# Performance work log

Hardware: AMD Instinct MI355X
Metric: run time of the kernel (lower is better)

The kernel has to match this reference:

```python
import jax, jax.numpy as jnp
import numpy as np

N_NODES = 100000
N_EDGES = 3200000
IN_FEAT = 512
HIDDEN = 256
N_CLASS = 40


def setup_inputs() -> dict:
    key = jax.random.key(0)
    ks = jax.random.split(key, 6)
    x = jax.random.normal(ks[0], (N_NODES, IN_FEAT), dtype=jnp.float32)
    w1 = jax.random.uniform(ks[1], (IN_FEAT, HIDDEN), dtype=jnp.float32)
    b1 = jnp.zeros((HIDDEN,), dtype=jnp.float32)
    w2 = jax.random.uniform(ks[2], (HIDDEN, N_CLASS), dtype=jnp.float32)
    b2 = jnp.zeros((N_CLASS,), dtype=jnp.float32)
    edge_val = jax.random.uniform(ks[3], (N_EDGES,), dtype=jnp.float32)
    edge_row = jax.random.randint(ks[4], (N_EDGES,), 0, N_NODES, dtype=jnp.int32)
    edge_col = jax.random.randint(ks[5], (N_EDGES,), 0, N_NODES, dtype=jnp.int32)
    return {"x": x, "w1": w1, "b1": b1, "w2": w2, "b2": b2,
            "edge_val": edge_val, "edge_row": edge_row, "edge_col": edge_col}


def _graph_conv(h, w, b, edge_val, edge_row, edge_col, n_nodes):
    # dense transform: [N, d_in] @ [d_in, d_out]
    support = h @ w
    # sparse adj @ support via gather + segment_sum (COO SpMM)
    msgs = edge_val[:, None] * support[edge_col]          # [E, d_out]
    agg = jax.ops.segment_sum(msgs, edge_row, num_segments=n_nodes)
    return agg + b


def reference(x, w1, b1, w2, b2, edge_val, edge_row, edge_col):
    n = x.shape[0]
    h = jax.nn.relu(_graph_conv(x, w1, b1, edge_val, edge_row, edge_col, n))
    # dropout is identity in eval mode (training=False)
    out = _graph_conv(h, w2, b2, edge_val, edge_row, edge_col, n)
    return jax.nn.log_softmax(out, axis=1)
```

## Files before the change

kernel.cpp:

```cpp
#include <hip/hip_runtime.h>
#include <cstdint>
#include <cstddef>

#define N_NODES 100000
#define N_EDGES 3200000
#define IN_FEAT 512
#define HIDDEN  256
#define N_CLASS 40

#define N_BUCKETS 196
#define SC_CHUNK 4096
#define N_SC_BLOCKS 782

#define OFF_SUPPORT1 ((size_t)0)
#define OFF_H        ((size_t)51200000)
#define OFF_SUPPORT2 ((size_t)102400000)
#define OFF_W1T      ((size_t)118400000)
#define OFF_RPTR     ((size_t)118662144)
#define OFF_BCNT     ((size_t)119062272)
#define OFF_BBASE    ((size_t)119063296)
#define OFF_BCUR     ((size_t)119064320)
#define OFF_BINNED   ((size_t)119065344)
#define OFF_SEDGE    ((size_t)144665344)

typedef __attribute__((ext_vector_type(8))) short short8x;
typedef __attribute__((ext_vector_type(4))) float f32x4;

static __device__ __forceinline__ unsigned short f2bf(float f) {
  unsigned u = __float_as_uint(f);
  unsigned r = (u + 0x7FFFu + ((u >> 16) & 1u)) >> 16;
  return (unsigned short)r;
}
static __device__ __forceinline__ float bf2f(unsigned short s) {
  return __uint_as_float(((unsigned)s) << 16);
}

__global__ __launch_bounds__(256) void k_bincnt(const int* __restrict__ erow,
                                                int* __restrict__ bcnt) {
  __shared__ int lh[256];
  lh[threadIdx.x] = 0;
  __syncthreads();
  int i = blockIdx.x * blockDim.x + threadIdx.x;
  int stride = gridDim.x * blockDim.x;
  for (; i < N_EDGES; i += stride) atomicAdd(&lh[erow[i] >> 9], 1);
  __syncthreads();
  if (threadIdx.x < N_BUCKETS) atomicAdd(&bcnt[threadIdx.x], lh[threadIdx.x]);
}

__global__ __launch_bounds__(256) void k_binscan(const int* __restrict__ bcnt,
                                                 int* __restrict__ bbase,
                                                 int* __restrict__ bcur,
                                                 int* __restrict__ rptr) {
  __shared__ int s[256];
  int t = threadIdx.x;
  int v = (t < N_BUCKETS) ? bcnt[t] : 0;
  s[t] = v;
  __syncthreads();
  for (int off = 1; off < 256; off <<= 1) {
    int y = (t >= off) ? s[t - off] : 0;
    __syncthreads();
    s[t] += y;
    __syncthreads();
  }
  if (t < N_BUCKETS) {
    int e = s[t] - v;
    bbase[t] = e;
    bcur[t] = e;
  }
  if (t == 0) {
    bbase[N_BUCKETS] = N_EDGES;
    rptr[N_NODES] = N_EDGES;
  }
}

__global__ __launch_bounds__(256) void k_binscatter(const int* __restrict__ erow,
                                                    const int* __restrict__ ecol,
                                                    const float* __restrict__ eval,
                                                    int* __restrict__ bcur,
                                                    int2* __restrict__ binned) {
  __shared__ int lcnt[256];
  __shared__ int lcur[256];
  const int t = threadIdx.x;
  const int base = blockIdx.x * SC_CHUNK;
  lcnt[t] = 0;
  __syncthreads();
  int rows[16], cols[16], vals[16];
#pragma unroll
  for (int e = 0; e < 16; e++) {
    int i = base + t + e * 256;
    if (i < N_EDGES) {
      rows[e] = erow[i];
      cols[e] = ecol[i];
      vals[e] = __float_as_int(eval[i]);
      atomicAdd(&lcnt[rows[e] >> 9], 1);
    } else {
      rows[e] = -1;
    }
  }
  __syncthreads();
  if (t < N_BUCKETS) lcur[t] = atomicAdd(&bcur[t], lcnt[t]);
  __syncthreads();
#pragma unroll
  for (int e = 0; e < 16; e++) {
    if (rows[e] >= 0) {
      int bkt = rows[e] >> 9;
      int p = atomicAdd(&lcur[bkt], 1);
      binned[p] = make_int2(((rows[e] & 511) << 17) | cols[e], vals[e]);
    }
  }
}

__global__ __launch_bounds__(256) void k_bucket_csr(const int2* __restrict__ binned,
                                                    const int* __restrict__ bbase,
                                                    int* __restrict__ rptr,
                                                    int2* __restrict__ sedge) {
  const int b = blockIdx.x;
  const int t = threadIdx.x;
  __shared__ int cnt[512];
  __shared__ int excl[512];
  __shared__ int s[256];
  cnt[t] = 0;
  cnt[t + 256] = 0;
  __syncthreads();
  const int ebase = bbase[b];
  const int ecnt = bbase[b + 1] - ebase;
  for (int i = t; i < ecnt; i += 256)
    atomicAdd(&cnt[((unsigned)binned[ebase + i].x) >> 17], 1);
  __syncthreads();
  int c0 = cnt[2 * t], c1 = cnt[2 * t + 1];
  s[t] = c0 + c1;
  __syncthreads();
  for (int off = 1; off < 256; off <<= 1) {
    int y = (t >= off) ? s[t - off] : 0;
    __syncthreads();
    s[t] += y;
    __syncthreads();
  }
  int e = s[t] - (c0 + c1);
  excl[2 * t] = e;
  excl[2 * t + 1] = e + c0;
  __syncthreads();
  for (int i = t; i < 512; i += 256) {
    int node = b * 512 + i;
    if (node < N_NODES) rptr[node] = ebase + excl[i];
  }
  __syncthreads();
  for (int i = t; i < ecnt; i += 256) {
    int2 e2 = binned[ebase + i];
    int lrow = ((unsigned)e2.x) >> 17;
    int col = e2.x & 0x1FFFF;
    int p = atomicAdd(&excl[lrow], 1);
    sedge[ebase + p] = make_int2(col, e2.y);
  }
}

__global__ __launch_bounds__(256) void k_prep_w(const float* __restrict__ W,
                                                unsigned short* __restrict__ Wt) {
  int tid = blockIdx.x * 256 + threadIdx.x;
  int n = tid & 255;
  int k = tid >> 8;
  Wt[(size_t)n * IN_FEAT + k] = f2bf(W[(size_t)k * HIDDEN + n]);
}

__global__ __launch_bounds__(256) void k_gemm1(const float* __restrict__ X,
                                               const unsigned short* __restrict__ Wt,
                                               unsigned short* __restrict__ C) {
  __shared__ short As[128 * 32];
  __shared__ short Bs[128 * 32];
  const int t = threadIdx.x;
  const int wave = t >> 6, lane = t & 63;
  const int q = lane >> 4, r = lane & 15;
  const int wm = (wave >> 1) * 64, wn = (wave & 1) * 64;
  const int m0 = blockIdx.x * 128;
  const int n0 = blockIdx.y * 128;

  f32x4 acc[4][4];
#pragma unroll
  for (int mi = 0; mi < 4; mi++)
#pragma unroll
    for (int ni = 0; ni < 4; ni++) acc[mi][ni] = (f32x4){0.f, 0.f, 0.f, 0.f};

  for (int k0 = 0; k0 < IN_FEAT; k0 += 32) {
#pragma unroll
    for (int i = 0; i < 2; i++) {
      int cidx = t + i * 256;
      int row = cidx >> 2;
      int ko = (cidx & 3) * 8;
      int gr = m0 + row;
      if (gr > N_NODES - 1) gr = N_NODES - 1;
      const float4* src = (const float4*)&X[(size_t)gr * IN_FEAT + k0 + ko];
      float4 x0 = src[0], x1 = src[1];
      short8x a;
      a[0] = (short)f2bf(x0.x); a[1] = (short)f2bf(x0.y);
      a[2] = (short)f2bf(x0.z); a[3] = (short)f2bf(x0.w);
      a[4] = (short)f2bf(x1.x); a[5] = (short)f2bf(x1.y);
      a[6] = (short)f2bf(x1.z); a[7] = (short)f2bf(x1.w);
      *(short8x*)&As[row * 32 + ko] = a;
    }
#pragma unroll
    for (int i = 0; i < 2; i++) {
      int cidx = t + i * 256;
      int row = cidx >> 2;
      int ko = (cidx & 3) * 8;
      short8x b = *(const short8x*)&Wt[(size_t)(n0 + row) * IN_FEAT + k0 + ko];
      *(short8x*)&Bs[row * 32 + ko] = b;
    }
    __syncthreads();
    short8x af[4], bf[4];
#pragma unroll
    for (int mi = 0; mi < 4; mi++)
      af[mi] = *(const short8x*)&As[(wm + mi * 16 + r) * 32 + q * 8];
#pragma unroll
    for (int ni = 0; ni < 4; ni++)
      bf[ni] = *(const short8x*)&Bs[(wn + ni * 16 + r) * 32 + q * 8];
#pragma unroll
    for (int mi = 0; mi < 4; mi++)
#pragma unroll
      for (int ni = 0; ni < 4; ni++)
        acc[mi][ni] = __builtin_amdgcn_mfma_f32_16x16x32_bf16(af[mi], bf[ni],
                                                              acc[mi][ni], 0, 0, 0);
    __syncthreads();
  }
#pragma unroll
  for (int mi = 0; mi < 4; mi++) {
#pragma unroll
    for (int ni = 0; ni < 4; ni++) {
#pragma unroll
      for (int reg = 0; reg < 4; reg++) {
        int row = m0 + wm + mi * 16 + q * 4 + reg;
        int col = n0 + wn + ni * 16 + r;
        if (row < N_NODES)
          C[(size_t)row * HIDDEN + col] = f2bf(acc[mi][ni][reg]);
      }
    }
  }
}

__global__ __launch_bounds__(256) void k_spmm1(const unsigned short* __restrict__ S,
                                               const int* __restrict__ rptr,
                                               const int2* __restrict__ sedge,
                                               const float* __restrict__ b1,
                                               unsigned short* __restrict__ H) {
  const int wid = (blockIdx.x * blockDim.x + threadIdx.x) >> 6;
  const int lane = threadIdx.x & 63;
  int e0 = rptr[wid], e1 = rptr[wid + 1];
  float a0 = 0.f, a1 = 0.f, a2 = 0.f, a3 = 0.f;
  for (int base = e0; base < e1; base += 64) {
    int rem = min(64, e1 - base);
    int c = 0;
    float v = 0.f;
    if (lane < rem) {
      int2 e = sedge[base + lane];
      c = e.x;
      v = __int_as_float(e.y);
    }
    for (int j = 0; j < rem; j++) {
      int cj = __shfl(c, j);
      float vj = __shfl(v, j);
      ushort4 s4 = *(const ushort4*)&S[(size_t)cj * HIDDEN + lane * 4];
      a0 += vj * bf2f(s4.x);
      a1 += vj * bf2f(s4.y);
      a2 += vj * bf2f(s4.z);
      a3 += vj * bf2f(s4.w);
    }
  }
  const float4 bb = *(const float4*)&b1[lane * 4];
  ushort4 o;
  o.x = f2bf(fmaxf(a0 + bb.x, 0.f));
  o.y = f2bf(fmaxf(a1 + bb.y, 0.f));
  o.z = f2bf(fmaxf(a2 + bb.z, 0.f));
  o.w = f2bf(fmaxf(a3 + bb.w, 0.f));
  *(ushort4*)&H[(size_t)wid * HIDDEN + lane * 4] = o;
}

__global__ __launch_bounds__(256) void k_gemm2(const unsigned short* __restrict__ H,
                                               const float* __restrict__ W2,
                                               float* __restrict__ S2) {
  __shared__ __align__(16) float Ws[HIDDEN][N_CLASS];
  __shared__ float Hs[256][33];
  const int t = threadIdx.x;
  const int r0 = blockIdx.x * 256;

#pragma unroll
  for (int i = 0; i < 10; i++) {
    int qq = t + i * 256;
    float4 w = *(const float4*)&W2[(size_t)qq * 4];
    *(float4*)&((float*)Ws)[(size_t)qq * 4] = w;
  }

  float acc[N_CLASS];
#pragma unroll
  for (int n = 0; n < N_CLASS; n++) acc[n] = 0.f;

  for (int kc = 0; kc < HIDDEN; kc += 32) {
    __syncthreads();
#pragma unroll
    for (int i = 0; i < 8; i++) {
      int qq = t + i * 256;
      int row = qq >> 3;
      int kv = (qq & 7) * 4;
      int grow = r0 + row;
      if (grow > N_NODES - 1) grow = N_NODES - 1;
      ushort4 hv = *(const ushort4*)&H[(size_t)grow * HIDDEN + kc + kv];
      Hs[row][kv + 0] = bf2f(hv.x);
      Hs[row][kv + 1] = bf2f(hv.y);
      Hs[row][kv + 2] = bf2f(hv.z);
      Hs[row][kv + 3] = bf2f(hv.w);
    }
    __syncthreads();
    const float4* Wsv = (const float4*)Ws;
#pragma unroll
    for (int k = 0; k < 32; k++) {
      float hk = Hs[t][k];
      int kg = kc + k;
#pragma unroll
      for (int n4 = 0; n4 < 10; n4++) {
        float4 w = Wsv[kg * 10 + n4];
        acc[n4 * 4 + 0] += hk * w.x;
        acc[n4 * 4 + 1] += hk * w.y;
        acc[n4 * 4 + 2] += hk * w.z;
        acc[n4 * 4 + 3] += hk * w.w;
      }
    }
  }
  int row = r0 + t;
  if (row < N_NODES) {
#pragma unroll
    for (int n4 = 0; n4 < 10; n4++) {
      float4 o = {acc[n4 * 4 + 0], acc[n4 * 4 + 1], acc[n4 * 4 + 2], acc[n4 * 4 + 3]};
      *(float4*)&S2[(size_t)row * N_CLASS + n4 * 4] = o;
    }
  }
}

__global__ __launch_bounds__(256) void k_spmm2(const float* __restrict__ S2,
                                               const int* __restrict__ rptr,
                                               const int2* __restrict__ sedge,
                                               const float* __restrict__ b2,
                                               float* __restrict__ out) {
  const int wid = (blockIdx.x * blockDim.x + threadIdx.x) >> 6;
  const int lane = threadIdx.x & 63;
  const bool act = lane < N_CLASS;
  const int f = act ? lane : 0;
  int e0 = rptr[wid], e1 = rptr[wid + 1];
  float acc = 0.f;
  for (int base = e0; base < e1; base += 64) {
    int rem = min(64, e1 - base);
    int c = 0;
    float v = 0.f;
    if (lane < rem) {
      int2 e = sedge[base + lane];
      c = e.x;
      v = __int_as_float(e.y);
    }
    for (int j = 0; j < rem; j++) {
      int cj = __shfl(c, j);
      float vj = __shfl(v, j);
      if (act) acc += vj * S2[(size_t)cj * N_CLASS + f];
    }
  }
  float x = act ? (acc + b2[f]) : -INFINITY;
  float m = x;
#pragma unroll
  for (int o = 32; o > 0; o >>= 1) m = fmaxf(m, __shfl_xor(m, o));
  float ex = act ? expf(x - m) : 0.f;
  float s = ex;
#pragma unroll
  for (int o = 32; o > 0; o >>= 1) s += __shfl_xor(s, o);
  if (act) out[(size_t)wid * N_CLASS + lane] = (x - m) - logf(s);
}

extern "C" void kernel_launch(void* const* d_in, const int* in_sizes, int n_in,
                              void* d_out, int out_size, void* d_ws, size_t ws_size,
                              hipStream_t stream) {
  const float* x    = (const float*)d_in[0];
  const float* w1   = (const float*)d_in[1];
  const float* b1   = (const float*)d_in[2];
  const float* w2   = (const float*)d_in[3];
  const float* b2   = (const float*)d_in[4];
  const float* eval = (const float*)d_in[5];
  const int*   erow = (const int*)d_in[6];
  const int*   ecol = (const int*)d_in[7];
  float* out = (float*)d_out;

  char* ws = (char*)d_ws;
  unsigned short* support1 = (unsigned short*)(ws + OFF_SUPPORT1);
  unsigned short* h        = (unsigned short*)(ws + OFF_H);
  float* support2 = (float*)(ws + OFF_SUPPORT2);
  unsigned short* w1t = (unsigned short*)(ws + OFF_W1T);
  int*   rptr   = (int*)(ws + OFF_RPTR);
  int*   bcnt   = (int*)(ws + OFF_BCNT);
  int*   bbase  = (int*)(ws + OFF_BBASE);
  int*   bcur   = (int*)(ws + OFF_BCUR);
  int2*  binned = (int2*)(ws + OFF_BINNED);
  int2*  sedge  = (int2*)(ws + OFF_SEDGE);

  hipMemsetAsync(bcnt, 0, N_BUCKETS * 4, stream);
  k_prep_w<<<512, 256, 0, stream>>>(w1, w1t);
  k_bincnt<<<512, 256, 0, stream>>>(erow, bcnt);
  k_binscan<<<1, 256, 0, stream>>>(bcnt, bbase, bcur, rptr);
  k_binscatter<<<N_SC_BLOCKS, 256, 0, stream>>>(erow, ecol, eval, bcur, binned);
  k_bucket_csr<<<N_BUCKETS, 256, 0, stream>>>(binned, bbase, rptr, sedge);

  k_gemm1<<<dim3((N_NODES + 127) / 128, HIDDEN / 128), 256, 0, stream>>>(x, w1t, support1);
  k_spmm1<<<N_NODES / 4, 256, 0, stream>>>(support1, rptr, sedge, b1, h);

  k_gemm2<<<(N_NODES + 255) / 256, 256, 0, stream>>>(h, w2, support2);
  k_spmm2<<<N_NODES / 4, 256, 0, stream>>>(support2, rptr, sedge, b2, out);
}
```

Measured before the change: 957.0 us.

## Chunk support1 features for L2-resident SpMM gathers; widen GEMM1 tile to full hidden

```diff
diff --git a/kernel.cpp b/kernel.cpp
--- a/kernel.cpp
+++ b/kernel.cpp
@@ -11,6 +11,9 @@
 #define N_BUCKETS 196
 #define SC_CHUNK 4096
 #define N_SC_BLOCKS 782
+
+#define S1_NCHUNKS 16
+#define S1_CHUNK_ELEMS ((size_t)N_NODES * 16)
 
 #define OFF_SUPPORT1 ((size_t)0)
 #define OFF_H        ((size_t)51200000)
@@ -166,19 +169,19 @@
                                                const unsigned short* __restrict__ Wt,
                                                unsigned short* __restrict__ C) {
   __shared__ short As[128 * 32];
-  __shared__ short Bs[128 * 32];
+  __shared__ short Bs[256 * 32];
   const int t = threadIdx.x;
   const int wave = t >> 6, lane = t & 63;
   const int q = lane >> 4, r = lane & 15;
-  const int wm = (wave >> 1) * 64, wn = (wave & 1) * 64;
+  const int wm = (wave >> 1) * 64;
+  const int wn = (wave & 1) * 128;
   const int m0 = blockIdx.x * 128;
-  const int n0 = blockIdx.y * 128;
-
-  f32x4 acc[4][4];
+
+  f32x4 acc[4][8];
 #pragma unroll
   for (int mi = 0; mi < 4; mi++)
 #pragma unroll
-    for (int ni = 0; ni < 4; ni++) acc[mi][ni] = (f32x4){0.f, 0.f, 0.f, 0.f};
+    for (int ni = 0; ni < 8; ni++) acc[mi][ni] = (f32x4){0.f, 0.f, 0.f, 0.f};
 
   for (int k0 = 0; k0 < IN_FEAT; k0 += 32) {
 #pragma unroll
@@ -198,25 +201,25 @@
       *(short8x*)&As[row * 32 + ko] = a;
     }
 #pragma unroll
-    for (int i = 0; i < 2; i++) {
+    for (int i = 0; i < 4; i++) {
       int cidx = t + i * 256;
       int row = cidx >> 2;
       int ko = (cidx & 3) * 8;
-      short8x b = *(const short8x*)&Wt[(size_t)(n0 + row) * IN_FEAT + k0 + ko];
+      short8x b = *(const short8x*)&Wt[(size_t)row * IN_FEAT + k0 + ko];
       *(short8x*)&Bs[row * 32 + ko] = b;
     }
     __syncthreads();
-    short8x af[4], bf[4];
+    short8x af[4], bf[8];
 #pragma unroll
     for (int mi = 0; mi < 4; mi++)
       af[mi] = *(const short8x*)&As[(wm + mi * 16 + r) * 32 + q * 8];
 #pragma unroll
-    for (int ni = 0; ni < 4; ni++)
+    for (int ni = 0; ni < 8; ni++)
       bf[ni] = *(const short8x*)&Bs[(wn + ni * 16 + r) * 32 + q * 8];
 #pragma unroll
     for (int mi = 0; mi < 4; mi++)
 #pragma unroll
-      for (int ni = 0; ni < 4; ni++)
+      for (int ni = 0; ni < 8; ni++)
         acc[mi][ni] = __builtin_amdgcn_mfma_f32_16x16x32_bf16(af[mi], bf[ni],
                                                               acc[mi][ni], 0, 0, 0);
     __syncthreads();
@@ -224,13 +227,14 @@
 #pragma unroll
   for (int mi = 0; mi < 4; mi++) {
 #pragma unroll
-    for (int ni = 0; ni < 4; ni++) {
+    for (int ni = 0; ni < 8; ni++) {
+      int chunk = (wn >> 4) + ni;
 #pragma unroll
       for (int reg = 0; reg < 4; reg++) {
         int row = m0 + wm + mi * 16 + q * 4 + reg;
-        int col = n0 + wn + ni * 16 + r;
         if (row < N_NODES)
-          C[(size_t)row * HIDDEN + col] = f2bf(acc[mi][ni][reg]);
+          C[(size_t)chunk * S1_CHUNK_ELEMS + (size_t)row * 16 + r] =
+              f2bf(acc[mi][ni][reg]);
       }
     }
   }
@@ -241,12 +245,16 @@
                                                const int2* __restrict__ sedge,
                                                const float* __restrict__ b1,
                                                unsigned short* __restrict__ H) {
-  const int wid = (blockIdx.x * blockDim.x + threadIdx.x) >> 6;
+  const int node = (blockIdx.x * blockDim.x + threadIdx.x) >> 6;
+  const int chunk = blockIdx.y;
   const int lane = threadIdx.x & 63;
-  int e0 = rptr[wid], e1 = rptr[wid + 1];
-  float a0 = 0.f, a1 = 0.f, a2 = 0.f, a3 = 0.f;
+  const int e8 = lane >> 3;
+  const int f2 = lane & 7;
+  const unsigned short* Sc = S + (size_t)chunk * S1_CHUNK_ELEMS;
+  int e0 = rptr[node], e1 = rptr[node + 1];
+  float a0 = 0.f, a1 = 0.f;
   for (int base = e0; base < e1; base += 64) {
-    int rem = min(64, e1 - base);
+    int rem = e1 - base;
     int c = 0;
     float v = 0.f;
     if (lane < rem) {
@@ -254,23 +262,29 @@
       c = e.x;
       v = __int_as_float(e.y);
     }
-    for (int j = 0; j < rem; j++) {
-      int cj = __shfl(c, j);
-      float vj = __shfl(v, j);
-      ushort4 s4 = *(const ushort4*)&S[(size_t)cj * HIDDEN + lane * 4];
-      a0 += vj * bf2f(s4.x);
-      a1 += vj * bf2f(s4.y);
-      a2 += vj * bf2f(s4.z);
-      a3 += vj * bf2f(s4.w);
-    }
-  }
-  const float4 bb = *(const float4*)&b1[lane * 4];
-  ushort4 o;
-  o.x = f2bf(fmaxf(a0 + bb.x, 0.f));
-  o.y = f2bf(fmaxf(a1 + bb.y, 0.f));
-  o.z = f2bf(fmaxf(a2 + bb.z, 0.f));
-  o.w = f2bf(fmaxf(a3 + bb.w, 0.f));
-  *(ushort4*)&H[(size_t)wid * HIDDEN + lane * 4] = o;
+#pragma unroll
+    for (int j = 0; j < 8; j++) {
+      int idx = j * 8 + e8;
+      int cj = __shfl(c, idx);
+      float vj = __shfl(v, idx);
+      ushort2 s2 = *(const ushort2*)&Sc[(size_t)cj * 16 + f2 * 2];
+      a0 += vj * bf2f(s2.x);
+      a1 += vj * bf2f(s2.y);
+    }
+  }
+#pragma unroll
+  for (int off = 8; off < 64; off <<= 1) {
+    a0 += __shfl_xor(a0, off);
+    a1 += __shfl_xor(a1, off);
+  }
+  if (e8 == 0) {
+    int fbase = chunk * 16 + f2 * 2;
+    float2 bb = *(const float2*)&b1[fbase];
+    ushort2 o;
+    o.x = f2bf(fmaxf(a0 + bb.x, 0.f));
+    o.y = f2bf(fmaxf(a1 + bb.y, 0.f));
+    *(ushort2*)&H[(size_t)node * HIDDEN + fbase] = o;
+  }
 }
 
 __global__ __launch_bounds__(256) void k_gemm2(const unsigned short* __restrict__ H,
@@ -402,8 +416,8 @@
   k_binscatter<<<N_SC_BLOCKS, 256, 0, stream>>>(erow, ecol, eval, bcur, binned);
   k_bucket_csr<<<N_BUCKETS, 256, 0, stream>>>(binned, bbase, rptr, sedge);
 
-  k_gemm1<<<dim3((N_NODES + 127) / 128, HIDDEN / 128), 256, 0, stream>>>(x, w1t, support1);
-  k_spmm1<<<N_NODES / 4, 256, 0, stream>>>(support1, rptr, sedge, b1, h);
+  k_gemm1<<<dim3((N_NODES + 127) / 128, 1), 256, 0, stream>>>(x, w1t, support1);
+  k_spmm1<<<dim3(N_NODES / 4, S1_NCHUNKS), 256, 0, stream>>>(support1, rptr, sedge, b1, h);
 
   k_gemm2<<<(N_NODES + 255) / 256, 256, 0, stream>>>(h, w2, support2);
   k_spmm2<<<N_NODES / 4, 256, 0, stream>>>(support2, rptr, sedge, b2, out);
```

Result: slower. 1.180 ms (+23.3%).
